# Kernel tuning notes

Measured on AMD Instinct MI355X. Metric: run time of the kernel, lower is better.

Reference implementation:

```python
import jax, jax.numpy as jnp
import numpy as np

TOKENS = 8192      # batch*seq flattened
D_IN = 2048        # in_features (power of 2 for Hadamard)
D_OUT = 8192       # out_features

try:
    FP8 = jnp.float8_e4m3fn
except AttributeError:
    FP8 = None


def fwht(x):
    """Normalized fast Walsh-Hadamard transform over last dim (power of 2)."""
    orig_shape = x.shape
    n = orig_shape[-1]
    x = x.reshape(-1, n)
    h = 1
    while h < n:
        x = x.reshape(-1, n // (2 * h), 2, h)
        a = x[..., 0, :]
        b = x[..., 1, :]
        x = jnp.stack([a + b, a - b], axis=-2).reshape(-1, n)
        h *= 2
    return (x * (1.0 / np.sqrt(n))).reshape(orig_shape)


def setup_inputs() -> dict:
    key = jax.random.key(0)
    kx, kw, kb = jax.random.split(key, 3)
    x = jax.random.normal(kx, (TOKENS, D_IN), dtype=jnp.float32)
    # Weight is stored in fp8 e4m3 (quantized in the Hadamard domain);
    # we materialize its dequantized fp32 values for the reference math.
    w = jax.random.normal(kw, (D_OUT, D_IN), dtype=jnp.float32) * 0.02
    if FP8 is not None:
        w = w.astype(FP8).astype(jnp.float32)  # simulate fp8 storage round-trip
    b = jax.random.normal(kb, (D_OUT,), dtype=jnp.float32) * 0.01
    return {"x": x, "weight": w, "bias": b}


def reference(x, weight, bias):
    # use_hadamard=True: rotate activations into the Hadamard domain
    # (weight was quantized in that domain), then fp8-dequant GEMM + bias.
    x_h = fwht(x)                               # [T, D_IN]
    out = jnp.einsum('td,od->to', x_h, weight)  # [T, D_OUT]
    return out + bias[None, :]
```

## Files before the change

kernel.cpp:

```cpp
#include <hip/hip_runtime.h>
#include <hip/hip_bf16.h>
#include <stdint.h>

#define TOKENS 8192
#define D_IN   2048
#define D_OUT  8192

typedef __attribute__((ext_vector_type(8))) short short8;
typedef __attribute__((ext_vector_type(4))) float floatx4;

__device__ __forceinline__ void async_copy16(const void* g, void* l) {
    __builtin_amdgcn_global_load_lds((const __attribute__((address_space(1))) void*)g,
                                     (__attribute__((address_space(3))) void*)l,
                                     16, 0, 0);
}

__device__ __forceinline__ void fwht8(float* e) {
#pragma unroll
    for (int s = 1; s < 8; s <<= 1) {
#pragma unroll
        for (int j = 0; j < 8; ++j) {
            if ((j & s) == 0) {
                float a = e[j], b = e[j | s];
                e[j]     = a + b;
                e[j | s] = a - b;
            }
        }
    }
}

__global__ __launch_bounds__(256) void fwht_kernel(const float* __restrict__ x,
                                                   __hip_bfloat16* __restrict__ xh) {
    __shared__ float row[D_IN];
    const int r = blockIdx.x;
    const int t = threadIdx.x;
    const float* xr = x + (size_t)r * D_IN;

    float e[8];
#pragma unroll
    for (int j = 0; j < 8; ++j) e[j] = xr[t + 256 * j];
    fwht8(e);
#pragma unroll
    for (int j = 0; j < 8; ++j) row[t + 256 * j] = e[j];
    __syncthreads();

    float f[8];
#pragma unroll
    for (int j = 0; j < 8; ++j) f[j] = row[8 * t + j];
    fwht8(f);
#pragma unroll
    for (int m = 1; m <= 16; m <<= 1) {
#pragma unroll
        for (int j = 0; j < 8; ++j) {
            float v = __shfl_xor(f[j], m, 64);
            f[j] = (t & m) ? (v - f[j]) : (f[j] + v);
        }
    }

    const float scale = 0.02209708691207961f;
    __hip_bfloat16 ob[8];
#pragma unroll
    for (int j = 0; j < 8; ++j) ob[j] = __float2bfloat16(f[j] * scale);
    __hip_bfloat16* orow = xh + (size_t)r * D_IN + 8 * t;
    *reinterpret_cast<int4*>(orow) = *reinterpret_cast<int4*>(ob);
}

__global__ __launch_bounds__(256) void wconv_kernel(const float* __restrict__ w,
                                                    __hip_bfloat16* __restrict__ wb) {
    const size_t i = ((size_t)blockIdx.x * 256 + threadIdx.x) * 8;
    float4 a = *reinterpret_cast<const float4*>(w + i);
    float4 b = *reinterpret_cast<const float4*>(w + i + 4);
    __hip_bfloat16 ob[8];
    ob[0] = __float2bfloat16(a.x); ob[1] = __float2bfloat16(a.y);
    ob[2] = __float2bfloat16(a.z); ob[3] = __float2bfloat16(a.w);
    ob[4] = __float2bfloat16(b.x); ob[5] = __float2bfloat16(b.y);
    ob[6] = __float2bfloat16(b.z); ob[7] = __float2bfloat16(b.w);
    *reinterpret_cast<int4*>(wb + i) = *reinterpret_cast<int4*>(ob);
}

__global__ __launch_bounds__(256) void gemm_kernel(const __hip_bfloat16* __restrict__ A,
                                                   const __hip_bfloat16* __restrict__ B,
                                                   const float* __restrict__ bias,
                                                   float* __restrict__ C) {
    __shared__ __hip_bfloat16 sA[128 * 32];
    __shared__ __hip_bfloat16 sB[128 * 32];

    const int tid  = threadIdx.x;
    const int wave = tid >> 6;
    const int lane = tid & 63;
    const int bm = blockIdx.y;
    const int bn = blockIdx.x;

    const int wm = wave & 1;
    const int wn = wave >> 1;
    const int lane16 = lane & 15;
    const int lgrp   = lane >> 4;

    floatx4 acc[4][4];
#pragma unroll
    for (int i = 0; i < 4; ++i)
#pragma unroll
        for (int j = 0; j < 4; ++j) acc[i][j] = 0;

    const int c0 = (wave * 2 + 0) * 64 + lane;
    const int c1 = (wave * 2 + 1) * 64 + lane;
    const int rA0 = c0 >> 2, kc0 = c0 & 3;
    const int rA1 = c1 >> 2, kc1 = c1 & 3;

    const __hip_bfloat16* gA0 = A + (size_t)(bm * 128 + rA0) * D_IN + kc0 * 8;
    const __hip_bfloat16* gA1 = A + (size_t)(bm * 128 + rA1) * D_IN + kc1 * 8;
    const __hip_bfloat16* gB0 = B + (size_t)(bn * 128 + rA0) * D_IN + kc0 * 8;
    const __hip_bfloat16* gB1 = B + (size_t)(bn * 128 + rA1) * D_IN + kc1 * 8;
    __hip_bfloat16* lA0 = sA + c0 * 8;
    __hip_bfloat16* lA1 = sA + c1 * 8;
    __hip_bfloat16* lB0 = sB + c0 * 8;
    __hip_bfloat16* lB1 = sB + c1 * 8;

    for (int k0 = 0; k0 < D_IN; k0 += 32) {
        async_copy16(gA0 + k0, lA0);
        async_copy16(gA1 + k0, lA1);
        async_copy16(gB0 + k0, lB0);
        async_copy16(gB1 + k0, lB1);
        __syncthreads();

        short8 af[4], bf[4];
#pragma unroll
        for (int i = 0; i < 4; ++i) {
            af[i] = *reinterpret_cast<const short8*>(sA + (wm * 64 + i * 16 + lane16) * 32 + lgrp * 8);
            bf[i] = *reinterpret_cast<const short8*>(sB + (wn * 64 + i * 16 + lane16) * 32 + lgrp * 8);
        }
#pragma unroll
        for (int i = 0; i < 4; ++i)
#pragma unroll
            for (int j = 0; j < 4; ++j)
                acc[i][j] = __builtin_amdgcn_mfma_f32_16x16x32_bf16(af[i], bf[j], acc[i][j], 0, 0, 0);
        __syncthreads();
    }

    float bv[4];
#pragma unroll
    for (int j = 0; j < 4; ++j) bv[j] = bias[bn * 128 + wn * 64 + j * 16 + lane16];

#pragma unroll
    for (int i = 0; i < 4; ++i) {
        const int rbase = bm * 128 + wm * 64 + i * 16 + lgrp * 4;
#pragma unroll
        for (int j = 0; j < 4; ++j) {
            const int col = bn * 128 + wn * 64 + j * 16 + lane16;
#pragma unroll
            for (int r = 0; r < 4; ++r) {
                C[(size_t)(rbase + r) * D_OUT + col] = acc[i][j][r] + bv[j];
            }
        }
    }
}

extern "C" void kernel_launch(void* const* d_in, const int* in_sizes, int n_in,
                              void* d_out, int out_size, void* d_ws, size_t ws_size,
                              hipStream_t stream) {
    const float* x    = (const float*)d_in[0];
    const float* w    = (const float*)d_in[1];
    const float* bias = (const float*)d_in[2];
    float* out = (float*)d_out;

    __hip_bfloat16* xh = (__hip_bfloat16*)d_ws;
    __hip_bfloat16* wb = xh + (size_t)TOKENS * D_IN;

    fwht_kernel<<<TOKENS, 256, 0, stream>>>(x, xh);
    wconv_kernel<<<(D_OUT * D_IN / 8) / 256, 256, 0, stream>>>(w, wb);
    gemm_kernel<<<dim3(D_OUT / 128, TOKENS / 128), 256, 0, stream>>>(xh, wb, bias, out);
}
```

Baseline: 639.6 us.

## Pre-swizzle weights into MFMA fragment order and stream B via registers

The weight conversion kernel now writes bf16 weights in a per-wave MFMA fragment layout, so the GEMM loads B operands directly from global memory into registers with prefetch and no LDS staging. A is double-buffered in LDS and loaded asynchronously one k-step ahead. Block indices are remapped into grouped tiles for L2 reuse, and output stores are nontemporal. This aims to cut LDS traffic, hide load latency and improve cache locality, but it adds register pressure and relies on global loads of B keeping up with the MFMA work.

```diff
diff --git a/kernel.cpp b/kernel.cpp
--- a/kernel.cpp
+++ b/kernel.cpp
@@ -65,31 +65,45 @@
     *reinterpret_cast<int4*>(orow) = *reinterpret_cast<int4*>(ob);
 }
 
-__global__ __launch_bounds__(256) void wconv_kernel(const float* __restrict__ w,
-                                                    __hip_bfloat16* __restrict__ wb) {
-    const size_t i = ((size_t)blockIdx.x * 256 + threadIdx.x) * 8;
-    float4 a = *reinterpret_cast<const float4*>(w + i);
-    float4 b = *reinterpret_cast<const float4*>(w + i + 4);
+__global__ __launch_bounds__(256) void wconv_swz_kernel(const float* __restrict__ w,
+                                                        __hip_bfloat16* __restrict__ wbs) {
+    const int tid  = threadIdx.x;
+    const int wave = tid >> 6;
+    const int lane = tid & 63;
+    const int W    = blockIdx.x * 4 + wave;
+    const int n16  = W >> 6;
+    const int kb   = W & 63;
+    const int l16  = lane & 15;
+    const int lgrp = lane >> 4;
+
+    const float* src = w + (size_t)(n16 * 16 + l16) * D_IN + kb * 32 + lgrp * 8;
+    float4 a = reinterpret_cast<const float4*>(src)[0];
+    float4 b = reinterpret_cast<const float4*>(src)[1];
     __hip_bfloat16 ob[8];
     ob[0] = __float2bfloat16(a.x); ob[1] = __float2bfloat16(a.y);
     ob[2] = __float2bfloat16(a.z); ob[3] = __float2bfloat16(a.w);
     ob[4] = __float2bfloat16(b.x); ob[5] = __float2bfloat16(b.y);
     ob[6] = __float2bfloat16(b.z); ob[7] = __float2bfloat16(b.w);
-    *reinterpret_cast<int4*>(wb + i) = *reinterpret_cast<int4*>(ob);
+    *reinterpret_cast<int4*>(wbs + (size_t)W * 512 + lane * 8) = *reinterpret_cast<int4*>(ob);
 }
 
 __global__ __launch_bounds__(256) void gemm_kernel(const __hip_bfloat16* __restrict__ A,
-                                                   const __hip_bfloat16* __restrict__ B,
+                                                   const __hip_bfloat16* __restrict__ Bs,
                                                    const float* __restrict__ bias,
                                                    float* __restrict__ C) {
-    __shared__ __hip_bfloat16 sA[128 * 32];
-    __shared__ __hip_bfloat16 sB[128 * 32];
+    __shared__ __hip_bfloat16 sA[2][128 * 32];
 
     const int tid  = threadIdx.x;
     const int wave = tid >> 6;
     const int lane = tid & 63;
-    const int bm = blockIdx.y;
-    const int bn = blockIdx.x;
+
+    const int bid = blockIdx.x;
+    const int x   = bid & 7;
+    const int s   = bid >> 3;
+    const int st  = s >> 6;
+    const int i2  = s & 63;
+    const int bm  = st * 8 + (i2 & 7);
+    const int bn  = x * 8 + (i2 >> 3);
 
     const int wm = wave & 1;
     const int wn = wave >> 1;
@@ -106,34 +120,48 @@
     const int c1 = (wave * 2 + 1) * 64 + lane;
     const int rA0 = c0 >> 2, kc0 = c0 & 3;
     const int rA1 = c1 >> 2, kc1 = c1 & 3;
-
     const __hip_bfloat16* gA0 = A + (size_t)(bm * 128 + rA0) * D_IN + kc0 * 8;
     const __hip_bfloat16* gA1 = A + (size_t)(bm * 128 + rA1) * D_IN + kc1 * 8;
-    const __hip_bfloat16* gB0 = B + (size_t)(bn * 128 + rA0) * D_IN + kc0 * 8;
-    const __hip_bfloat16* gB1 = B + (size_t)(bn * 128 + rA1) * D_IN + kc1 * 8;
-    __hip_bfloat16* lA0 = sA + c0 * 8;
-    __hip_bfloat16* lA1 = sA + c1 * 8;
-    __hip_bfloat16* lB0 = sB + c0 * 8;
-    __hip_bfloat16* lB1 = sB + c1 * 8;
-
-    for (int k0 = 0; k0 < D_IN; k0 += 32) {
-        async_copy16(gA0 + k0, lA0);
-        async_copy16(gA1 + k0, lA1);
-        async_copy16(gB0 + k0, lB0);
-        async_copy16(gB1 + k0, lB1);
-        __syncthreads();
-
-        short8 af[4], bf[4];
-#pragma unroll
-        for (int i = 0; i < 4; ++i) {
-            af[i] = *reinterpret_cast<const short8*>(sA + (wm * 64 + i * 16 + lane16) * 32 + lgrp * 8);
-            bf[i] = *reinterpret_cast<const short8*>(sB + (wn * 64 + i * 16 + lane16) * 32 + lgrp * 8);
-        }
+
+    const __hip_bfloat16* gB[4];
+#pragma unroll
+    for (int j = 0; j < 4; ++j)
+        gB[j] = Bs + (size_t)(bn * 8 + wn * 4 + j) * 64 * 512 + lane * 8;
+
+    async_copy16(gA0, sA[0] + c0 * 8);
+    async_copy16(gA1, sA[0] + c1 * 8);
+    short8 bcur[4], bnext[4];
+#pragma unroll
+    for (int j = 0; j < 4; ++j)
+        bcur[j] = *reinterpret_cast<const short8*>(gB[j]);
+    __syncthreads();
+
+#pragma unroll 4
+    for (int kb = 0; kb < 64; ++kb) {
+        if (kb < 63) {
+            async_copy16(gA0 + (kb + 1) * 32, sA[(kb + 1) & 1] + c0 * 8);
+            async_copy16(gA1 + (kb + 1) * 32, sA[(kb + 1) & 1] + c1 * 8);
+        }
+        const int kn = (kb < 63) ? kb + 1 : 63;
+#pragma unroll
+        for (int j = 0; j < 4; ++j)
+            bnext[j] = *reinterpret_cast<const short8*>(gB[j] + kn * 512);
+
+        const __hip_bfloat16* sab = sA[kb & 1];
+        short8 af[4];
 #pragma unroll
         for (int i = 0; i < 4; ++i)
+            af[i] = *reinterpret_cast<const short8*>(sab + (wm * 64 + i * 16 + lane16) * 32 + lgrp * 8);
+
+#pragma unroll
+        for (int i = 0; i < 4; ++i)
 #pragma unroll
             for (int j = 0; j < 4; ++j)
-                acc[i][j] = __builtin_amdgcn_mfma_f32_16x16x32_bf16(af[i], bf[j], acc[i][j], 0, 0, 0);
+                acc[i][j] = __builtin_amdgcn_mfma_f32_16x16x32_bf16(af[i], bcur[j], acc[i][j], 0, 0, 0);
+
+#pragma unroll
+        for (int j = 0; j < 4; ++j) bcur[j] = bnext[j];
+
         __syncthreads();
     }
 
@@ -149,7 +177,8 @@
             const int col = bn * 128 + wn * 64 + j * 16 + lane16;
 #pragma unroll
             for (int r = 0; r < 4; ++r) {
-                C[(size_t)(rbase + r) * D_OUT + col] = acc[i][j][r] + bv[j];
+                float v = acc[i][j][r] + bv[j];
+                __builtin_nontemporal_store(v, &C[(size_t)(rbase + r) * D_OUT + col]);
             }
         }
     }
@@ -163,10 +192,10 @@
     const float* bias = (const float*)d_in[2];
     float* out = (float*)d_out;
 
-    __hip_bfloat16* xh = (__hip_bfloat16*)d_ws;
-    __hip_bfloat16* wb = xh + (size_t)TOKENS * D_IN;
+    __hip_bfloat16* xh  = (__hip_bfloat16*)d_ws;
+    __hip_bfloat16* wbs = xh + (size_t)TOKENS * D_IN;
 
     fwht_kernel<<<TOKENS, 256, 0, stream>>>(x, xh);
-    wconv_kernel<<<(D_OUT * D_IN / 8) / 256, 256, 0, stream>>>(w, wb);
-    gemm_kernel<<<dim3(D_OUT / 128, TOKENS / 128), 256, 0, stream>>>(xh, wb, bias, out);
-}
+    wconv_swz_kernel<<<(D_OUT / 16) * (D_IN / 32) / 4, 256, 0, stream>>>(w, wbs);
+    gemm_kernel<<<4096, 256, 0, stream>>>(xh, wbs, bias, out);
+}
```

After: 665.1 us. +4.0%, slower.
